# Kernel tuning notes

Hardware: AMD Instinct MI355X
Metric: run time of the kernel (lower is better)

## Reference

```python
import jax, jax.numpy as jnp
import numpy as np
from jax import lax

B, C, K, H, W = 32, 256, 64, 64, 64  # batch, num_channels, num_corr_channels, spatial
IN = C + K  # enc input channels = 320
EPS = 1e-5


def setup_inputs() -> dict:
    key = jax.random.key(0)
    ks = jax.random.split(key, 20)
    n = lambda k, s, sc=0.05: jax.random.normal(k, s, dtype=jnp.float32) * sc
    return {
        "z": jax.random.normal(ks[0], (B, C, K), dtype=jnp.float32),
        "x": jax.random.normal(ks[1], (B, C, H, W), dtype=jnp.float32),
        "d": jax.random.normal(ks[2], (B, C, H, W), dtype=jnp.float32),
        # ConvBlock: depthwise [IN,1,3,3] + pointwise [C,IN]
        "dw_w": n(ks[3], (IN, 1, 3, 3), 0.1),
        "dw_b": n(ks[4], (IN,)),
        "pw_w": n(ks[5], (C, IN), 0.05),
        "pw_b": n(ks[6], (C,)),
        # BatchNorm2d (inference-mode running stats)
        "bn_gamma": 1.0 + n(ks[7], (C,)),
        "bn_beta": n(ks[8], (C,)),
        "bn_mean": n(ks[9], (C,)),
        "bn_var": 0.5 + jax.random.uniform(ks[10], (C,), dtype=jnp.float32),
        # SelfAttention: 1x1 conv projections + q/k/v linears
        "inp_w": n(ks[11], (C, C)), "inp_b": n(ks[12], (C,)),
        "q_w": n(ks[13], (C, C)), "q_b": n(ks[14], (C,)),
        "k_w": n(ks[15], (C, C)), "k_b": n(ks[16], (C,)),
        "v_w": n(ks[17], (C, C)), "v_b": n(ks[18], (C,)),
        "op_w": n(ks[19], (C, C)), "op_b": jnp.zeros((C,), jnp.float32),
    }


def reference(z, x, d, dw_w, dw_b, pw_w, pw_b, bn_gamma, bn_beta, bn_mean, bn_var,
              inp_w, inp_b, q_w, q_b, k_w, k_b, v_w, v_b, op_w, op_b):
    b, c, h, w = x.shape
    # correlation: z^T @ x_flat -> [b, K, h*w] -> [b, K, h, w]
    s = jnp.einsum('bck,bcn->bkn', z, x.reshape(b, c, h * w)).reshape(b, -1, h, w)
    s = jnp.concatenate([s, d], axis=1)  # [b, C+K, h, w]
    # depthwise 3x3 (pad 1) + pointwise 1x1
    s = lax.conv_general_dilated(s, dw_w, (1, 1), [(1, 1), (1, 1)],
                                 dimension_numbers=('NCHW', 'OIHW', 'NCHW'),
                                 feature_group_count=s.shape[1]) + dw_b[:, None, None]
    s = jnp.einsum('bihw,oi->bohw', s, pw_w) + pw_b[:, None, None]
    # BN (inference) + ReLU
    s = (s - bn_mean[:, None, None]) * lax.rsqrt(bn_var[:, None, None] + EPS)
    s = jnp.maximum(s * bn_gamma[:, None, None] + bn_beta[:, None, None], 0.0)
    # channel self-attention
    px = jnp.einsum('bchw,oc->bohw', s, inp_w) + inp_b[:, None, None]
    flat = px.reshape(b, c, h * w).transpose(0, 2, 1)  # [b, n, c]
    q = flat @ q_w.T + q_b
    k = flat @ k_w.T + k_b
    v = flat @ v_w.T + v_b
    score = jnp.einsum('bnc,bnd->bcd', q, k) / (c ** 0.5)  # [b, c, c]
    att = jax.nn.softmax(score, axis=2)
    weighted = jnp.einsum('bnc,bcd->bnd', v, att)  # values @ attention
    wt = weighted.transpose(0, 2, 1).reshape(b, c, h, w)
    out = jnp.einsum('bchw,oc->bohw', wt, op_w) + op_b[:, None, None]
    return out + s
```

## Files before the change

kernel.cpp:

```cpp
#include <hip/hip_runtime.h>

static constexpr int B_ = 32, C_ = 256, K_ = 64, H_ = 64, W_ = 64;
static constexpr int N_ = H_ * W_;
static constexpr int IN_ = C_ + K_;

__device__ __forceinline__ short f2bs(float f) {
  unsigned u = __builtin_bit_cast(unsigned, f);
  u += 0x7fffu + ((u >> 16) & 1u);
  return (short)(u >> 16);
}
__device__ __forceinline__ float bs2f(short s) {
  unsigned u = ((unsigned)(unsigned short)s) << 16;
  return __builtin_bit_cast(float, u);
}

typedef __attribute__((ext_vector_type(8))) short s8v;
typedef __attribute__((ext_vector_type(4))) short s4v;
typedef __attribute__((ext_vector_type(4))) float f4v;

static constexpr long long OB_XT   = 0;
static constexpr long long OB_ZT   = 67108864LL;
static constexpr long long OB_DWS  = 0;
static constexpr long long OB_DT   = 83886080LL;
static constexpr long long OB_PX   = 83886080LL;
static constexpr long long OB_CORR = 150994944LL;
static constexpr long long OB_G    = 150994944LL;
static constexpr long long OB_T1   = 159383552LL;
static constexpr long long OB_S    = 167772160LL;
static constexpr long long OB_PXT  = 234881024LL;
static constexpr long long OB_ATT  = 301989888LL;
static constexpr long long OB_M2   = OB_ATT + 8388608LL;
static constexpr long long OB_M3   = OB_M2 + 8388608LL;
static constexpr long long OB_MISC = OB_M3 + 8388608LL;
static constexpr long long OB_PWW  = OB_MISC;
static constexpr long long OB_INPW = OB_PWW + 262144LL;
static constexpr long long OB_M3B  = OB_INPW + 262144LL;
static constexpr long long OB_R    = OB_M3B + 4194304LL;
static constexpr long long OB_U    = OB_R + 32768LL;
static constexpr long long OB_W2   = OB_U + 32768LL;
static constexpr long long OB_M2B  = OB_W2 + 32768LL;
static constexpr long long OB_B3   = OB_M2B + 32768LL;
static constexpr long long OB_BNS  = OB_B3 + 32768LL;
static constexpr long long OB_BNH  = OB_BNS + 2048LL;

__device__ __forceinline__ void gload16(const void* g, void* l) {
  __builtin_amdgcn_global_load_lds((const __attribute__((address_space(1))) void*)g,
                                   (__attribute__((address_space(3))) void*)l, 16, 0, 0);
}

template <int BN, int SPLIT, int EPI>
__global__ __launch_bounds__(256) void mgemm(
    const short* __restrict__ A, int lda, long long sA,
    const short* __restrict__ Bt, int ldb, long long sB,
    void* __restrict__ Cv, int ldc, long long sC,
    int Kd,
    const float* __restrict__ biasc, const float* __restrict__ shf,
    const float* __restrict__ biasr,
    const short* __restrict__ resT, int ldrt, long long sRT,
    short* __restrict__ outT, int ldt, long long sT)
{
  constexpr int JT = BN / 32;
  __shared__ short As[128 * 32];
  __shared__ short Bs[BN * 32];

  const int t = threadIdx.x;
  const int wv = t >> 6;
  const int lane = t & 63, quad = lane >> 4, lr = lane & 15;
  const int wm = wv >> 1, wn = wv & 1;
  const int m_off = wm * 64, n_off = wn * (BN / 2);

  const int n0 = blockIdx.x * BN;
  const int m0 = blockIdx.y * 128;
  const int bz = (SPLIT == 1) ? blockIdx.z : (blockIdx.z / SPLIT);
  const int sp = (SPLIT == 1) ? 0 : (blockIdx.z % SPLIT);
  const int koff = sp * Kd;

  A += (long long)bz * sA;
  Bt += (long long)bz * sB;

  const int arow = t >> 2;
  const int acol = (t & 3) << 3;

  f4v acc[4][JT];
#pragma unroll
  for (int i = 0; i < 4; ++i)
#pragma unroll
    for (int j = 0; j < JT; ++j) acc[i][j] = (f4v)0.f;

  for (int k0 = 0; k0 < Kd; k0 += 32) {
#pragma unroll
    for (int rr = 0; rr < 2; ++rr) {
      const short* gp = A + (long long)(m0 + rr * 64 + arow) * lda + koff + k0 + acol;
      gload16(gp, (char*)As + rr * 4096 + wv * 1024);
    }
#pragma unroll
    for (int rr = 0; rr < BN / 64; ++rr) {
      const short* gp = Bt + (long long)(n0 + rr * 64 + arow) * ldb + koff + k0 + acol;
      gload16(gp, (char*)Bs + rr * 4096 + wv * 1024);
    }
    __syncthreads();

    s8v af[4], bfv[JT];
#pragma unroll
    for (int i = 0; i < 4; ++i)
      af[i] = *(const s8v*)&As[(m_off + i * 16 + lr) * 32 + quad * 8];
#pragma unroll
    for (int j = 0; j < JT; ++j)
      bfv[j] = *(const s8v*)&Bs[(n_off + j * 16 + lr) * 32 + quad * 8];
#pragma unroll
    for (int i = 0; i < 4; ++i)
#pragma unroll
      for (int j = 0; j < JT; ++j)
        acc[i][j] = __builtin_amdgcn_mfma_f32_16x16x32_bf16(af[i], bfv[j], acc[i][j], 0, 0, 0);
    __syncthreads();
  }

  float* Cf = (float*)Cv;
  short* Cb = (short*)Cv;
  if (EPI & 1) Cb += (long long)bz * sC; else Cf += (long long)bz * sC;
  if (EPI & 16) resT += (long long)bz * sRT;
  if (EPI & 32) outT += (long long)bz * sT;

#pragma unroll
  for (int i = 0; i < 4; ++i) {
    const int mb = m0 + m_off + i * 16 + quad * 4;
#pragma unroll
    for (int j = 0; j < JT; ++j) {
      const int n = n0 + n_off + j * 16 + lr;
      float vr[4];
#pragma unroll
      for (int r = 0; r < 4; ++r) {
        float v = acc[i][j][r];
        if (EPI & 2) v += biasc[n];
        if (EPI & 4) v = fmaxf(fmaf(v, biasc[n], shf[n]), 0.f);
        if (EPI & 8) v += biasr[bz * 256 + mb + r];
        vr[r] = v;
      }
      if (EPI & 16) {
        s4v rv = *(const s4v*)(resT + (long long)n * ldrt + mb);
#pragma unroll
        for (int r = 0; r < 4; ++r) vr[r] += bs2f(rv[r]);
      }
      if (EPI & 32) {
        s4v tv;
#pragma unroll
        for (int r = 0; r < 4; ++r) tv[r] = f2bs(vr[r]);
        *(s4v*)(outT + (long long)n * ldt + mb) = tv;
      }
#pragma unroll
      for (int r = 0; r < 4; ++r) {
        if (EPI & 64) atomicAdd(&Cf[(long long)(mb + r) * ldc + n], vr[r]);
        else if (EPI & 1) Cb[(long long)(mb + r) * ldc + n] = f2bs(vr[r]);
        else Cf[(long long)(mb + r) * ldc + n] = vr[r];
      }
    }
  }
}

__global__ __launch_bounds__(256) void tcast(const float* __restrict__ in,
                                             short* __restrict__ out,
                                             int R, int Cc, long long sIn, long long sOut)
{
  __shared__ float tile[32][33];
  const int b = blockIdx.z;
  const int r0 = blockIdx.y * 32, c0 = blockIdx.x * 32;
  in += (long long)b * sIn;
  out += (long long)b * sOut;
  const int tx = threadIdx.x & 31, ty = threadIdx.x >> 5;
#pragma unroll
  for (int i = 0; i < 32; i += 8)
    tile[ty + i][tx] = in[(long long)(r0 + ty + i) * Cc + c0 + tx];
  __syncthreads();
#pragma unroll
  for (int i = 0; i < 32; i += 8)
    out[(long long)(c0 + ty + i) * R + r0 + tx] = f2bs(tile[tx][ty + i]);
}

__global__ void castw(const float* __restrict__ in, short* __restrict__ out, long long n)
{
  long long i = (long long)blockIdx.x * 256 + threadIdx.x;
  if (i < n) out[i] = f2bs(in[i]);
}

__global__ __launch_bounds__(256) void dwconv3(const short* __restrict__ corr,
                                               const short* __restrict__ dt,
                                               const float* __restrict__ wgt,
                                               const float* __restrict__ bias,
                                               short* __restrict__ outp)
{
  __shared__ __align__(16) float wl[9 * IN_];
  __shared__ __align__(16) float bl[IN_];
  const int tid = threadIdx.x;
  for (int i = tid; i < 9 * IN_; i += 256) {
    const int ch = i / 9, tap = i % 9;
    wl[tap * IN_ + ch] = wgt[i];
  }
  for (int i = tid; i < IN_; i += 256) bl[i] = bias[i];
  __syncthreads();

  const int id = blockIdx.x * 256 + tid;
  const int b = blockIdx.y;
  const int cg = id % 40;
  const int pix = id / 40;
  const int y = pix >> 6, x = pix & 63;
  const int ch0 = cg * 8;

  const short* base;
  int ldch, c0;
  if (cg < 8) { base = corr + (long long)b * N_ * K_; ldch = K_; c0 = ch0; }
  else        { base = dt   + (long long)b * N_ * C_; ldch = C_; c0 = ch0 - K_; }

  float acc[8];
  {
    float4 bv0 = *(const float4*)&bl[ch0];
    float4 bv1 = *(const float4*)&bl[ch0 + 4];
    acc[0] = bv0.x; acc[1] = bv0.y; acc[2] = bv0.z; acc[3] = bv0.w;
    acc[4] = bv1.x; acc[5] = bv1.y; acc[6] = bv1.z; acc[7] = bv1.w;
  }

#pragma unroll
  for (int dy = -1; dy <= 1; ++dy) {
    const int yy = y + dy;
    if (yy < 0 || yy >= H_) continue;
#pragma unroll
    for (int dx = -1; dx <= 1; ++dx) {
      const int xx = x + dx;
      if (xx < 0 || xx >= W_) continue;
      const int tap = (dy + 1) * 3 + (dx + 1);
      s8v v = *(const s8v*)(base + (long long)(yy * W_ + xx) * ldch + c0);
      float4 wa = *(const float4*)&wl[tap * IN_ + ch0];
      float4 wb = *(const float4*)&wl[tap * IN_ + ch0 + 4];
      acc[0] = fmaf(wa.x, bs2f(v[0]), acc[0]);
      acc[1] = fmaf(wa.y, bs2f(v[1]), acc[1]);
      acc[2] = fmaf(wa.z, bs2f(v[2]), acc[2]);
      acc[3] = fmaf(wa.w, bs2f(v[3]), acc[3]);
      acc[4] = fmaf(wb.x, bs2f(v[4]), acc[4]);
      acc[5] = fmaf(wb.y, bs2f(v[5]), acc[5]);
      acc[6] = fmaf(wb.z, bs2f(v[6]), acc[6]);
      acc[7] = fmaf(wb.w, bs2f(v[7]), acc[7]);
    }
  }

  s8v o;
#pragma unroll
  for (int j = 0; j < 8; ++j) o[j] = f2bs(acc[j]);
  *(s8v*)(outp + ((long long)b * N_ + pix) * IN_ + ch0) = o;
}

__global__ void colsum(const short* __restrict__ px, float* __restrict__ r)
{
  const int b = blockIdx.y, c = threadIdx.x, chunk = blockIdx.x;
  const short* p = px + (long long)b * N_ * C_ + (long long)chunk * 512 * C_;
  float s = 0.f;
  for (int n = 0; n < 512; ++n) s += bs2f(p[(long long)n * C_ + c]);
  atomicAdd(&r[b * C_ + c], s);
}

template <int TA, int TB, int EPI>
__global__ __launch_bounds__(256) void gemm64(
    const float* __restrict__ A, int lda, long long sA,
    const float* __restrict__ B, int ldb, long long sB,
    float* __restrict__ Cout, int ldc, long long sC,
    int Kd, float alpha)
{
  const int n0 = blockIdx.x * 64;
  const int m0 = blockIdx.y * 64;
  const int bz = blockIdx.z;
  A += (long long)bz * sA;
  B += (long long)bz * sB;
  Cout += (long long)bz * sC;

  __shared__ __align__(16) float As[16][68];
  __shared__ __align__(16) float Bs[16][68];
  const int tid = threadIdx.x;
  const int tx = tid & 15, ty = tid >> 4;
  float acc[4][4] = {};

  for (int k0 = 0; k0 < Kd; k0 += 16) {
    if (TA == 0) {
      const int m = tid >> 2, k4 = (tid & 3) << 2;
      float4 v = *(const float4*)(A + (long long)(m0 + m) * lda + k0 + k4);
      As[k4 + 0][m] = v.x; As[k4 + 1][m] = v.y;
      As[k4 + 2][m] = v.z; As[k4 + 3][m] = v.w;
    } else {
      const int kk = tid >> 4, m4 = (tid & 15) << 2;
      *(float4*)&As[kk][m4] = *(const float4*)(A + (long long)(k0 + kk) * lda + m0 + m4);
    }
    if (TB == 0) {
      const int kk = tid >> 4, n4 = (tid & 15) << 2;
      *(float4*)&Bs[kk][n4] = *(const float4*)(B + (long long)(k0 + kk) * ldb + n0 + n4);
    } else {
      const int n = tid >> 2, k4 = (tid & 3) << 2;
      float4 v = *(const float4*)(B + (long long)(n0 + n) * ldb + k0 + k4);
      Bs[k4 + 0][n] = v.x; Bs[k4 + 1][n] = v.y;
      Bs[k4 + 2][n] = v.z; Bs[k4 + 3][n] = v.w;
    }
    __syncthreads();
#pragma unroll
    for (int kk = 0; kk < 16; ++kk) {
      float4 av = *(const float4*)&As[kk][ty << 2];
      float4 bv = *(const float4*)&Bs[kk][tx << 2];
      float a[4] = {av.x, av.y, av.z, av.w};
      float b[4] = {bv.x, bv.y, bv.z, bv.w};
#pragma unroll
      for (int i = 0; i < 4; ++i)
#pragma unroll
        for (int j = 0; j < 4; ++j) acc[i][j] = fmaf(a[i], b[j], acc[i][j]);
    }
    __syncthreads();
  }
#pragma unroll
  for (int i = 0; i < 4; ++i)
#pragma unroll
    for (int j = 0; j < 4; ++j) {
      float v = acc[i][j];
      if (EPI & 8) v *= alpha;
      Cout[(long long)(m0 + (ty << 2) + i) * ldc + n0 + (tx << 2) + j] = v;
    }
}

__global__ void bncoef(const float* __restrict__ pwb, const float* __restrict__ g,
                       const float* __restrict__ bt, const float* __restrict__ mn,
                       const float* __restrict__ vr, float* __restrict__ scl,
                       float* __restrict__ shf)
{
  const int c = threadIdx.x;
  const float inv = rsqrtf(vr[c] + 1e-5f);
  const float sc = g[c] * inv;
  scl[c] = sc;
  shf[c] = (pwb[c] - mn[c]) * sc + bt[c];
}

__global__ void uwker(const float* __restrict__ qw, const float* __restrict__ kw,
                      const float* __restrict__ r, float* __restrict__ u,
                      float* __restrict__ w)
{
  const int b = blockIdx.x, c = threadIdx.x;
  __shared__ float rl[256];
  rl[c] = r[b * C_ + c];
  __syncthreads();
  float su = 0.f, sw = 0.f;
  for (int f = 0; f < C_; ++f) {
    const float rv = rl[f];
    su = fmaf(qw[c * C_ + f], rv, su);
    sw = fmaf(kw[c * C_ + f], rv, sw);
  }
  u[b * C_ + c] = su;
  w[b * C_ + c] = sw;
}

__global__ void fixsoftmax(float* __restrict__ att, const float* __restrict__ u,
                           const float* __restrict__ w, const float* __restrict__ qb,
                           const float* __restrict__ kb)
{
  const int c = blockIdx.x, b = blockIdx.y, d = threadIdx.x;
  const long long base = ((long long)b * C_ + c) * (long long)C_;
  const float qbc = qb[c];
  float val = att[base + d] +
              0.0625f * (u[b * C_ + c] * kb[d] + qbc * w[b * C_ + d] +
                         (float)N_ * qbc * kb[d]);
  __shared__ float red[256];
  red[d] = val;
  __syncthreads();
  for (int k = 128; k > 0; k >>= 1) {
    if (d < k) red[d] = fmaxf(red[d], red[d + k]);
    __syncthreads();
  }
  const float mx = red[0];
  __syncthreads();
  const float e = expf(val - mx);
  red[d] = e;
  __syncthreads();
  for (int k = 128; k > 0; k >>= 1) {
    if (d < k) red[d] += red[d + k];
    __syncthreads();
  }
  att[base + d] = e / red[0];
}

__global__ void m2bker(const float* __restrict__ att, const float* __restrict__ vb,
                       float* __restrict__ m2b)
{
  const int b = blockIdx.x, d = threadIdx.x;
  const float* a = att + (long long)b * C_ * C_;
  float s = 0.f;
  for (int c = 0; c < C_; ++c) s = fmaf(a[c * C_ + d], vb[c], s);
  m2b[b * C_ + d] = s;
}

__global__ void b3ker(const float* __restrict__ opw, const float* __restrict__ m2b,
                      const float* __restrict__ opb, float* __restrict__ b3)
{
  const int b = blockIdx.x, o = threadIdx.x;
  __shared__ float m[256];
  m[o] = m2b[b * C_ + o];
  __syncthreads();
  float s = opb[o];
  for (int d = 0; d < C_; ++d) s = fmaf(opw[o * C_ + d], m[d], s);
  b3[b * C_ + o] = s;
}

extern "C" void kernel_launch(void* const* d_in, const int* in_sizes, int n_in,
                              void* d_out, int out_size, void* d_ws, size_t ws_size,
                              hipStream_t stream)
{
  (void)in_sizes; (void)n_in; (void)out_size; (void)ws_size;
  const float* z     = (const float*)d_in[0];
  const float* x     = (const float*)d_in[1];
  const float* dimg  = (const float*)d_in[2];
  const float* dw_w  = (const float*)d_in[3];
  const float* dw_b  = (const float*)d_in[4];
  const float* pw_w  = (const float*)d_in[5];
  const float* pw_b  = (const float*)d_in[6];
  const float* bn_g  = (const float*)d_in[7];
  const float* bn_b  = (const float*)d_in[8];
  const float* bn_m  = (const float*)d_in[9];
  const float* bn_v  = (const float*)d_in[10];
  const float* inp_w = (const float*)d_in[11];
  const float* inp_b = (const float*)d_in[12];
  const float* q_w   = (const float*)d_in[13];
  const float* q_b   = (const float*)d_in[14];
  const float* k_w   = (const float*)d_in[15];
  const float* k_b   = (const float*)d_in[16];
  const float* v_w   = (const float*)d_in[17];
  const float* v_b   = (const float*)d_in[18];
  const float* op_w  = (const float*)d_in[19];
  const float* op_b  = (const float*)d_in[20];
  float* out = (float*)d_out;

  char* ws = (char*)d_ws;
  short* xt    = (short*)(ws + OB_XT);
  short* zt    = (short*)(ws + OB_ZT);
  short* dws   = (short*)(ws + OB_DWS);
  short* dt    = (short*)(ws + OB_DT);
  short* px_b  = (short*)(ws + OB_PX);
  short* corr  = (short*)(ws + OB_CORR);
  float* G     = (float*)(ws + OB_G);
  float* T1    = (float*)(ws + OB_T1);
  short* s_b   = (short*)(ws + OB_S);
  short* pxT   = (short*)(ws + OB_PXT);
  float* att   = (float*)(ws + OB_ATT);
  float* M2    = (float*)(ws + OB_M2);
  float* M3    = (float*)(ws + OB_M3);
  short* pw_wb = (short*)(ws + OB_PWW);
  short* inp_wb= (short*)(ws + OB_INPW);
  short* M3b   = (short*)(ws + OB_M3B);
  float* r     = (float*)(ws + OB_R);
  float* u     = (float*)(ws + OB_U);
  float* w2    = (float*)(ws + OB_W2);
  float* m2b   = (float*)(ws + OB_M2B);
  float* b3    = (float*)(ws + OB_B3);
  float* bns   = (float*)(ws + OB_BNS);
  float* bnh   = (float*)(ws + OB_BNH);

  const long long sNC = (long long)N_ * C_;
  const long long sNK = (long long)N_ * K_;
  const long long sNI = (long long)N_ * IN_;
  const long long sCC = (long long)C_ * C_;

  bncoef<<<1, 256, 0, stream>>>(pw_b, bn_g, bn_b, bn_m, bn_v, bns, bnh);
  castw<<<(IN_ * C_ + 255) / 256, 256, 0, stream>>>(pw_w, pw_wb, IN_ * C_);
  castw<<<(C_ * C_ + 255) / 256, 256, 0, stream>>>(inp_w, inp_wb, C_ * C_);
  tcast<<<dim3(N_ / 32, C_ / 32, B_), 256, 0, stream>>>(x, xt, C_, N_, sNC, sNC);
  tcast<<<dim3(K_ / 32, C_ / 32, B_), 256, 0, stream>>>(z, zt, C_, K_, (long long)C_ * K_,
                                                        (long long)C_ * K_);
  tcast<<<dim3(N_ / 32, C_ / 32, B_), 256, 0, stream>>>(dimg, dt, C_, N_, sNC, sNC);

  mgemm<64, 1, 1><<<dim3(1, 32, B_), 256, 0, stream>>>(
      xt, C_, sNC, zt, C_, (long long)K_ * C_, corr, K_, sNK, C_,
      nullptr, nullptr, nullptr, nullptr, 0, 0, nullptr, 0, 0);

  dwconv3<<<dim3(N_ * 40 / 256, B_), 256, 0, stream>>>(corr, dt, dw_w, dw_b, dws);

  mgemm<128, 1, (1 | 4)><<<dim3(2, 32, B_), 256, 0, stream>>>(
      dws, IN_, sNI, pw_wb, IN_, 0, s_b, C_, sNC, IN_,
      bns, bnh, nullptr, nullptr, 0, 0, nullptr, 0, 0);

  mgemm<128, 1, (1 | 2 | 32)><<<dim3(2, 32, B_), 256, 0, stream>>>(
      s_b, C_, sNC, inp_wb, C_, 0, px_b, C_, sNC, C_,
      inp_b, nullptr, nullptr, nullptr, 0, 0, pxT, N_, sNC);

  hipMemsetAsync(r, 0, B_ * C_ * sizeof(float), stream);
  colsum<<<dim3(8, B_), 256, 0, stream>>>(px_b, r);

  hipMemsetAsync(G, 0, (size_t)B_ * C_ * C_ * sizeof(float), stream);
  mgemm<128, 8, 64><<<dim3(2, 2, B_ * 8), 256, 0, stream>>>(
      pxT, N_, sNC, pxT, N_, sNC, G, C_, sCC, N_ / 8,
      nullptr, nullptr, nullptr, nullptr, 0, 0, nullptr, 0, 0);

  uwker<<<B_, 256, 0, stream>>>(q_w, k_w, r, u, w2);

  gemm64<0, 0, 0><<<dim3(C_ / 64, C_ / 64, B_), 256, 0, stream>>>(
      q_w, C_, 0, G, C_, sCC, T1, C_, sCC, C_, 1.f);
  gemm64<0, 1, 8><<<dim3(C_ / 64, C_ / 64, B_), 256, 0, stream>>>(
      T1, C_, sCC, k_w, C_, 0, att, C_, sCC, C_, 0.0625f);

  fixsoftmax<<<dim3(C_, B_), 256, 0, stream>>>(att, u, w2, q_b, k_b);

  gemm64<1, 0, 0><<<dim3(C_ / 64, C_ / 64, B_), 256, 0, stream>>>(
      att, C_, sCC, v_w, C_, 0, M2, C_, sCC, C_, 1.f);
  m2bker<<<B_, 256, 0, stream>>>(att, v_b, m2b);
  gemm64<0, 0, 0><<<dim3(C_ / 64, C_ / 64, B_), 256, 0, stream>>>(
      op_w, C_, 0, M2, C_, sCC, M3, C_, sCC, C_, 1.f);
  b3ker<<<B_, 256, 0, stream>>>(op_w, m2b, op_b, b3);
  castw<<<((int)(B_ * sCC) + 255) / 256, 256, 0, stream>>>(M3, M3b, B_ * sCC);

  mgemm<128, 1, (8 | 16)><<<dim3(32, 2, B_), 256, 0, stream>>>(
      M3b, C_, sCC, px_b, C_, sNC, out, N_, sNC, C_,
      nullptr, nullptr, b3, s_b, C_, sNC, nullptr, 0, 0);
}
```

Measured before the change: 879.9 us.

## Move small CxC attention GEMMs to bf16 MFMA and tile depthwise conv over rows

Replaces the four fp32 SIMT gemm64 calls in the attention chain (q_w·G, ·k_w, att·v_w, op_w·M2) with the bf16 MFMA mgemm kernel. Pre-cast weights and a transposed attention matrix feed it, and G is split into hi/lo bf16 halves against a duplicated q_w to keep precision in the first product. The alpha scale moves into fixsoftmax, and the final M3 cast is dropped because mgemm writes bf16 directly. The depthwise conv now computes four output rows per thread, reusing the six loaded input rows and the hoisted weights. This adds several small cast and transpose launches, and lowers precision in the att/M2/M3 products.

```diff
diff --git a/kernel.cpp b/kernel.cpp
--- a/kernel.cpp
+++ b/kernel.cpp
@@ -25,7 +25,7 @@
 static constexpr long long OB_PX   = 83886080LL;
 static constexpr long long OB_CORR = 150994944LL;
 static constexpr long long OB_G    = 150994944LL;
-static constexpr long long OB_T1   = 159383552LL;
+static constexpr long long OB_GB2  = 159383552LL;
 static constexpr long long OB_S    = 167772160LL;
 static constexpr long long OB_PXT  = 234881024LL;
 static constexpr long long OB_ATT  = 301989888LL;
@@ -42,6 +42,14 @@
 static constexpr long long OB_B3   = OB_M2B + 32768LL;
 static constexpr long long OB_BNS  = OB_B3 + 32768LL;
 static constexpr long long OB_BNH  = OB_BNS + 2048LL;
+static constexpr long long OB_QW2  = OB_BNH + 2048LL;
+static constexpr long long OB_KWB  = OB_QW2 + 262144LL;
+static constexpr long long OB_VWB  = OB_KWB + 131072LL;
+static constexpr long long OB_OPWB = OB_VWB + 131072LL;
+static constexpr long long OB_T1B  = OB_OPWB + 131072LL;
+static constexpr long long OB_ATTT = OB_T1B + 4194304LL;
+static constexpr long long OB_M2T  = OB_ATTT + 4194304LL;
+static constexpr long long OB_VWT  = OB_M2T + 4194304LL;
 
 __device__ __forceinline__ void gload16(const void* g, void* l) {
   __builtin_amdgcn_global_load_lds((const __attribute__((address_space(1))) void*)g,
@@ -182,7 +190,38 @@
   if (i < n) out[i] = f2bs(in[i]);
 }
 
-__global__ __launch_bounds__(256) void dwconv3(const short* __restrict__ corr,
+__global__ void castw2(const float* __restrict__ a, const float* __restrict__ b,
+                       short* __restrict__ oa, short* __restrict__ ob)
+{
+  const int i = blockIdx.x * 256 + threadIdx.x;
+  const int sel = i >> 16, off = i & 65535;
+  const float* src = sel == 0 ? a : b;
+  short* dst = sel == 0 ? oa : ob;
+  dst[off] = f2bs(src[off]);
+}
+
+__global__ void qdup(const float* __restrict__ q, short* __restrict__ o)
+{
+  const int i = blockIdx.x * 256 + threadIdx.x;
+  const short v = f2bs(q[i]);
+  const int c = i >> 8, e = i & 255;
+  o[c * 512 + e] = v;
+  o[c * 512 + 256 + e] = v;
+}
+
+__global__ void ghilo(const float* __restrict__ G, short* __restrict__ g2)
+{
+  const long long i = (long long)blockIdx.x * 256 + threadIdx.x;
+  const float g = G[i];
+  const short h = f2bs(g);
+  const short l = f2bs(g - bs2f(h));
+  const long long row = i >> 8;
+  const int e = (int)(i & 255);
+  g2[row * 512 + e] = h;
+  g2[row * 512 + 256 + e] = l;
+}
+
+__global__ __launch_bounds__(256) void dwconv4(const short* __restrict__ corr,
                                                const short* __restrict__ dt,
                                                const float* __restrict__ wgt,
                                                const float* __restrict__ bias,
@@ -198,11 +237,12 @@
   for (int i = tid; i < IN_; i += 256) bl[i] = bias[i];
   __syncthreads();
 
-  const int id = blockIdx.x * 256 + tid;
+  const int g = blockIdx.x * 256 + tid;
   const int b = blockIdx.y;
-  const int cg = id % 40;
-  const int pix = id / 40;
-  const int y = pix >> 6, x = pix & 63;
+  const int cg = g % 40;
+  const int rest = g / 40;
+  const int x = rest & 63;
+  const int y0 = (rest >> 6) << 2;
   const int ch0 = cg * 8;
 
   const short* base;
@@ -210,41 +250,64 @@
   if (cg < 8) { base = corr + (long long)b * N_ * K_; ldch = K_; c0 = ch0; }
   else        { base = dt   + (long long)b * N_ * C_; ldch = C_; c0 = ch0 - K_; }
 
-  float acc[8];
+  float acc[4][8];
   {
     float4 bv0 = *(const float4*)&bl[ch0];
     float4 bv1 = *(const float4*)&bl[ch0 + 4];
-    acc[0] = bv0.x; acc[1] = bv0.y; acc[2] = bv0.z; acc[3] = bv0.w;
-    acc[4] = bv1.x; acc[5] = bv1.y; acc[6] = bv1.z; acc[7] = bv1.w;
-  }
-
-#pragma unroll
-  for (int dy = -1; dy <= 1; ++dy) {
-    const int yy = y + dy;
-    if (yy < 0 || yy >= H_) continue;
-#pragma unroll
-    for (int dx = -1; dx <= 1; ++dx) {
-      const int xx = x + dx;
-      if (xx < 0 || xx >= W_) continue;
-      const int tap = (dy + 1) * 3 + (dx + 1);
-      s8v v = *(const s8v*)(base + (long long)(yy * W_ + xx) * ldch + c0);
-      float4 wa = *(const float4*)&wl[tap * IN_ + ch0];
-      float4 wb = *(const float4*)&wl[tap * IN_ + ch0 + 4];
-      acc[0] = fmaf(wa.x, bs2f(v[0]), acc[0]);
-      acc[1] = fmaf(wa.y, bs2f(v[1]), acc[1]);
-      acc[2] = fmaf(wa.z, bs2f(v[2]), acc[2]);
-      acc[3] = fmaf(wa.w, bs2f(v[3]), acc[3]);
-      acc[4] = fmaf(wb.x, bs2f(v[4]), acc[4]);
-      acc[5] = fmaf(wb.y, bs2f(v[5]), acc[5]);
-      acc[6] = fmaf(wb.z, bs2f(v[6]), acc[6]);
-      acc[7] = fmaf(wb.w, bs2f(v[7]), acc[7]);
-    }
-  }
-
-  s8v o;
-#pragma unroll
-  for (int j = 0; j < 8; ++j) o[j] = f2bs(acc[j]);
-  *(s8v*)(outp + ((long long)b * N_ + pix) * IN_ + ch0) = o;
+#pragma unroll
+    for (int p = 0; p < 4; ++p) {
+      acc[p][0] = bv0.x; acc[p][1] = bv0.y; acc[p][2] = bv0.z; acc[p][3] = bv0.w;
+      acc[p][4] = bv1.x; acc[p][5] = bv1.y; acc[p][6] = bv1.z; acc[p][7] = bv1.w;
+    }
+  }
+
+#pragma unroll
+  for (int dx = -1; dx <= 1; ++dx) {
+    const int xx = x + dx;
+    if (xx < 0 || xx >= W_) continue;
+
+    float wv[3][8];
+#pragma unroll
+    for (int dy1 = 0; dy1 < 3; ++dy1) {
+      float4 wa = *(const float4*)&wl[(dy1 * 3 + (dx + 1)) * IN_ + ch0];
+      float4 wb = *(const float4*)&wl[(dy1 * 3 + (dx + 1)) * IN_ + ch0 + 4];
+      wv[dy1][0] = wa.x; wv[dy1][1] = wa.y; wv[dy1][2] = wa.z; wv[dy1][3] = wa.w;
+      wv[dy1][4] = wb.x; wv[dy1][5] = wb.y; wv[dy1][6] = wb.z; wv[dy1][7] = wb.w;
+    }
+
+    s8v v[6];
+#pragma unroll
+    for (int ri = 0; ri < 6; ++ri) {
+      const int yy = y0 - 1 + ri;
+      if (yy >= 0 && yy < H_)
+        v[ri] = *(const s8v*)(base + (long long)(yy * W_ + xx) * ldch + c0);
+      else
+        v[ri] = (s8v)0;
+    }
+
+#pragma unroll
+    for (int ri = 0; ri < 6; ++ri) {
+      float f[8];
+#pragma unroll
+      for (int j = 0; j < 8; ++j) f[j] = bs2f(v[ri][j]);
+#pragma unroll
+      for (int dy1 = 0; dy1 < 3; ++dy1) {
+        const int p = ri - dy1;
+        if (p < 0 || p > 3) continue;
+#pragma unroll
+        for (int j = 0; j < 8; ++j)
+          acc[p][j] = fmaf(wv[dy1][j], f[j], acc[p][j]);
+      }
+    }
+  }
+
+#pragma unroll
+  for (int p = 0; p < 4; ++p) {
+    s8v o;
+#pragma unroll
+    for (int j = 0; j < 8; ++j) o[j] = f2bs(acc[p][j]);
+    *(s8v*)(outp + ((long long)b * N_ + (y0 + p) * W_ + x) * IN_ + ch0) = o;
+  }
 }
 
 __global__ void colsum(const short* __restrict__ px, float* __restrict__ r)
@@ -256,69 +319,6 @@
   atomicAdd(&r[b * C_ + c], s);
 }
 
-template <int TA, int TB, int EPI>
-__global__ __launch_bounds__(256) void gemm64(
-    const float* __restrict__ A, int lda, long long sA,
-    const float* __restrict__ B, int ldb, long long sB,
-    float* __restrict__ Cout, int ldc, long long sC,
-    int Kd, float alpha)
-{
-  const int n0 = blockIdx.x * 64;
-  const int m0 = blockIdx.y * 64;
-  const int bz = blockIdx.z;
-  A += (long long)bz * sA;
-  B += (long long)bz * sB;
-  Cout += (long long)bz * sC;
-
-  __shared__ __align__(16) float As[16][68];
-  __shared__ __align__(16) float Bs[16][68];
-  const int tid = threadIdx.x;
-  const int tx = tid & 15, ty = tid >> 4;
-  float acc[4][4] = {};
-
-  for (int k0 = 0; k0 < Kd; k0 += 16) {
-    if (TA == 0) {
-      const int m = tid >> 2, k4 = (tid & 3) << 2;
-      float4 v = *(const float4*)(A + (long long)(m0 + m) * lda + k0 + k4);
-      As[k4 + 0][m] = v.x; As[k4 + 1][m] = v.y;
-      As[k4 + 2][m] = v.z; As[k4 + 3][m] = v.w;
-    } else {
-      const int kk = tid >> 4, m4 = (tid & 15) << 2;
-      *(float4*)&As[kk][m4] = *(const float4*)(A + (long long)(k0 + kk) * lda + m0 + m4);
-    }
-    if (TB == 0) {
-      const int kk = tid >> 4, n4 = (tid & 15) << 2;
-      *(float4*)&Bs[kk][n4] = *(const float4*)(B + (long long)(k0 + kk) * ldb + n0 + n4);
-    } else {
-      const int n = tid >> 2, k4 = (tid & 3) << 2;
-      float4 v = *(const float4*)(B + (long long)(n0 + n) * ldb + k0 + k4);
-      Bs[k4 + 0][n] = v.x; Bs[k4 + 1][n] = v.y;
-      Bs[k4 + 2][n] = v.z; Bs[k4 + 3][n] = v.w;
-    }
-    __syncthreads();
-#pragma unroll
-    for (int kk = 0; kk < 16; ++kk) {
-      float4 av = *(const float4*)&As[kk][ty << 2];
-      float4 bv = *(const float4*)&Bs[kk][tx << 2];
-      float a[4] = {av.x, av.y, av.z, av.w};
-      float b[4] = {bv.x, bv.y, bv.z, bv.w};
-#pragma unroll
-      for (int i = 0; i < 4; ++i)
-#pragma unroll
-        for (int j = 0; j < 4; ++j) acc[i][j] = fmaf(a[i], b[j], acc[i][j]);
-    }
-    __syncthreads();
-  }
-#pragma unroll
-  for (int i = 0; i < 4; ++i)
-#pragma unroll
-    for (int j = 0; j < 4; ++j) {
-      float v = acc[i][j];
-      if (EPI & 8) v *= alpha;
-      Cout[(long long)(m0 + (ty << 2) + i) * ldc + n0 + (tx << 2) + j] = v;
-    }
-}
-
 __global__ void bncoef(const float* __restrict__ pwb, const float* __restrict__ g,
                        const float* __restrict__ bt, const float* __restrict__ mn,
                        const float* __restrict__ vr, float* __restrict__ scl,
@@ -356,8 +356,7 @@
   const int c = blockIdx.x, b = blockIdx.y, d = threadIdx.x;
   const long long base = ((long long)b * C_ + c) * (long long)C_;
   const float qbc = qb[c];
-  float val = att[base + d] +
-              0.0625f * (u[b * C_ + c] * kb[d] + qbc * w[b * C_ + d] +
+  float val = 0.0625f * (att[base + d] + u[b * C_ + c] * kb[d] + qbc * w[b * C_ + d] +
                          (float)N_ * qbc * kb[d]);
   __shared__ float red[256];
   red[d] = val;
@@ -436,12 +435,11 @@
   short* px_b  = (short*)(ws + OB_PX);
   short* corr  = (short*)(ws + OB_CORR);
   float* G     = (float*)(ws + OB_G);
-  float* T1    = (float*)(ws + OB_T1);
+  short* Gb2   = (short*)(ws + OB_GB2);
   short* s_b   = (short*)(ws + OB_S);
   short* pxT   = (short*)(ws + OB_PXT);
   float* att   = (float*)(ws + OB_ATT);
-  float* M2    = (float*)(ws + OB_M2);
-  float* M3    = (float*)(ws + OB_M3);
+  short* M2scr = (short*)(ws + OB_M2);
   short* pw_wb = (short*)(ws + OB_PWW);
   short* inp_wb= (short*)(ws + OB_INPW);
   short* M3b   = (short*)(ws + OB_M3B);
@@ -452,6 +450,13 @@
   float* b3    = (float*)(ws + OB_B3);
   float* bns   = (float*)(ws + OB_BNS);
   float* bnh   = (float*)(ws + OB_BNH);
+  short* q_wb2 = (short*)(ws + OB_QW2);
+  short* k_wb  = (short*)(ws + OB_KWB);
+  short* op_wb = (short*)(ws + OB_OPWB);
+  short* T1b   = (short*)(ws + OB_T1B);
+  short* attT  = (short*)(ws + OB_ATTT);
+  short* M2T   = (short*)(ws + OB_M2T);
+  short* v_wT  = (short*)(ws + OB_VWT);
 
   const long long sNC = (long long)N_ * C_;
   const long long sNK = (long long)N_ * K_;
@@ -461,6 +466,9 @@
   bncoef<<<1, 256, 0, stream>>>(pw_b, bn_g, bn_b, bn_m, bn_v, bns, bnh);
   castw<<<(IN_ * C_ + 255) / 256, 256, 0, stream>>>(pw_w, pw_wb, IN_ * C_);
   castw<<<(C_ * C_ + 255) / 256, 256, 0, stream>>>(inp_w, inp_wb, C_ * C_);
+  qdup<<<256, 256, 0, stream>>>(q_w, q_wb2);
+  castw2<<<512, 256, 0, stream>>>(k_w, op_w, k_wb, op_wb);
+  tcast<<<dim3(8, 8, 1), 256, 0, stream>>>(v_w, v_wT, C_, C_, 0, 0);
   tcast<<<dim3(N_ / 32, C_ / 32, B_), 256, 0, stream>>>(x, xt, C_, N_, sNC, sNC);
   tcast<<<dim3(K_ / 32, C_ / 32, B_), 256, 0, stream>>>(z, zt, C_, K_, (long long)C_ * K_,
                                                         (long long)C_ * K_);
@@ -470,7 +478,7 @@
       xt, C_, sNC, zt, C_, (long long)K_ * C_, corr, K_, sNK, C_,
       nullptr, nullptr, nullptr, nullptr, 0, 0, nullptr, 0, 0);
 
-  dwconv3<<<dim3(N_ * 40 / 256, B_), 256, 0, stream>>>(corr, dt, dw_w, dw_b, dws);
+  dwconv4<<<dim3(160, B_), 256, 0, stream>>>(corr, dt, dw_w, dw_b, dws);
 
   mgemm<128, 1, (1 | 4)><<<dim3(2, 32, B_), 256, 0, stream>>>(
       dws, IN_, sNI, pw_wb, IN_, 0, s_b, C_, sNC, IN_,
@@ -488,22 +496,32 @@
       pxT, N_, sNC, pxT, N_, sNC, G, C_, sCC, N_ / 8,
       nullptr, nullptr, nullptr, nullptr, 0, 0, nullptr, 0, 0);
 
+  ghilo<<<8192, 256, 0, stream>>>(G, Gb2);
+
   uwker<<<B_, 256, 0, stream>>>(q_w, k_w, r, u, w2);
 
-  gemm64<0, 0, 0><<<dim3(C_ / 64, C_ / 64, B_), 256, 0, stream>>>(
-      q_w, C_, 0, G, C_, sCC, T1, C_, sCC, C_, 1.f);
-  gemm64<0, 1, 8><<<dim3(C_ / 64, C_ / 64, B_), 256, 0, stream>>>(
-      T1, C_, sCC, k_w, C_, 0, att, C_, sCC, C_, 0.0625f);
+  mgemm<128, 1, 1><<<dim3(2, 2, B_), 256, 0, stream>>>(
+      q_wb2, 512, 0, Gb2, 512, 256LL * 512, T1b, C_, sCC, 512,
+      nullptr, nullptr, nullptr, nullptr, 0, 0, nullptr, 0, 0);
+
+  mgemm<128, 1, 0><<<dim3(2, 2, B_), 256, 0, stream>>>(
+      T1b, C_, sCC, k_wb, C_, 0, att, C_, sCC, C_,
+      nullptr, nullptr, nullptr, nullptr, 0, 0, nullptr, 0, 0);
 
   fixsoftmax<<<dim3(C_, B_), 256, 0, stream>>>(att, u, w2, q_b, k_b);
 
-  gemm64<1, 0, 0><<<dim3(C_ / 64, C_ / 64, B_), 256, 0, stream>>>(
-      att, C_, sCC, v_w, C_, 0, M2, C_, sCC, C_, 1.f);
+  tcast<<<dim3(8, 8, B_), 256, 0, stream>>>(att, attT, C_, C_, sCC, sCC);
+
+  mgemm<128, 1, (1 | 32)><<<dim3(2, 2, B_), 256, 0, stream>>>(
+      attT, C_, sCC, v_wT, C_, 0, M2scr, C_, sCC, C_,
+      nullptr, nullptr, nullptr, nullptr, 0, 0, M2T, C_, sCC);
+
+  mgemm<128, 1, 1><<<dim3(2, 2, B_), 256, 0, stream>>>(
+      op_wb, C_, 0, M2T, C_, sCC, M3b, C_, sCC, C_,
+      nullptr, nullptr, nullptr, nullptr, 0, 0, nullptr, 0, 0);
+
   m2bker<<<B_, 256, 0, stream>>>(att, v_b, m2b);
-  gemm64<0, 0, 0><<<dim3(C_ / 64, C_ / 64, B_), 256, 0, stream>>>(
-      op_w, C_, 0, M2, C_, sCC, M3, C_, sCC, C_, 1.f);
   b3ker<<<B_, 256, 0, stream>>>(op_w, m2b, op_b, b3);
-  castw<<<((int)(B_ * sCC) + 255) / 256, 256, 0, stream>>>(M3, M3b, B_ * sCC);
 
   mgemm<128, 1, (8 | 16)><<<dim3(32, 2, B_), 256, 0, stream>>>(
       M3b, C_, sCC, px_b, C_, sNC, out, N_, sNC, C_,
```

New measurement: 853.3 us. 1.03x faster.
